# Kernel tuning notes

Measured on AMD Instinct MI355X. Metric: run time of the kernel, lower is better.

Reference implementation:

```python
import jax, jax.numpy as jnp
import numpy as np

N_NODES = 100000
N_EDGES = 1500000
N_REL = 3
HID = 256


def setup_inputs() -> dict:
    key = jax.random.key(0)
    ks = jax.random.split(key, 8)
    return {
        "feat_a": jax.random.normal(ks[0], (N_NODES, 256), dtype=jnp.float32),
        "feat_b": jax.random.normal(ks[1], (N_NODES, 384), dtype=jnp.float32),
        "Wp_a": jax.random.normal(ks[2], (256, HID), dtype=jnp.float32) * 0.03,
        "Wp_b": jax.random.normal(ks[3], (384, HID), dtype=jnp.float32) * 0.03,
        "Wr": jax.random.normal(ks[4], (N_REL, HID, HID), dtype=jnp.float32) * 0.06,
        "ln_gamma": jnp.ones((HID,), dtype=jnp.float32),
        "ln_beta": jnp.zeros((HID,), dtype=jnp.float32),
        "edge_weight": jax.random.uniform(ks[5], (N_EDGES,), dtype=jnp.float32),
        "edge_src": jax.random.randint(ks[6], (N_EDGES,), 0, N_NODES, dtype=jnp.int32),
        "edge_dst": jax.random.randint(ks[7], (N_EDGES,), 0, N_NODES, dtype=jnp.int32),
    }


def _layer_norm(x, gamma, beta, eps=1e-5):
    mu = jnp.mean(x, axis=-1, keepdims=True)
    var = jnp.mean(jnp.square(x - mu), axis=-1, keepdims=True)
    return (x - mu) * jax.lax.rsqrt(var + eps) * gamma + beta


def reference(feat_a, feat_b, Wp_a, Wp_b, Wr, ln_gamma, ln_beta,
              edge_weight, edge_src, edge_dst):
    # avg fusion of modality projections (bias-free linears), padding node zeroed
    h0 = 0.5 * (feat_a @ Wp_a + feat_b @ Wp_b)  # [N, H]
    h0 = h0.at[0].set(0.0)

    n = h0.shape[0]
    e_per_rel = edge_src.shape[0] // N_REL  # edges pre-sorted by relation id
    aggregated = jnp.zeros_like(h0)
    for r in range(N_REL):
        s = slice(r * e_per_rel, (r + 1) * e_per_rel)
        src, dst, w = edge_src[s], edge_dst[s], edge_weight[s]
        # gather -> relation linear -> weight scale  [E_r, H]
        msg = (h0[src] @ Wr[r]) * w[:, None]
        num = jax.ops.segment_sum(msg, dst, num_segments=n)
        den = jax.ops.segment_sum(w, dst, num_segments=n)
        aggregated = aggregated + num / jnp.maximum(den, 1e-8)[:, None]

    # dropout p=0 / eval -> identity; residual + LayerNorm, padding node zeroed
    h1 = _layer_norm(h0 + aggregated, ln_gamma, ln_beta)
    h1 = h1.at[0].set(0.0)
    return h1
```

## Files before the change

### kernel.cpp

```cpp
#include <hip/hip_runtime.h>

#define N_NODES 100000
#define HID 256
#define N_EDGES 1500000
#define N_REL 3
#define E_PER_REL (N_EDGES / N_REL)
#define NKEYS (N_REL * N_NODES)
#define KP 640
#define KR 768

#define SCAN_CHUNK 1024
#define NSCANBLK ((NKEYS + SCAN_CHUNK - 1) / SCAN_CHUNK)

typedef __attribute__((ext_vector_type(8))) short bf16x8;
typedef __attribute__((ext_vector_type(4))) float f32x4;

__device__ __forceinline__ short f2bf(float x) {
    union { float f; unsigned u; } v; v.f = x;
    unsigned r = v.u + 0x7fffu + ((v.u >> 16) & 1u);
    return (short)(r >> 16);
}
__device__ __forceinline__ float bf2f(short h) {
    union { unsigned u; float f; } v;
    v.u = ((unsigned)(unsigned short)h) << 16;
    return v.f;
}
__device__ __forceinline__ int xorf(int r) { return (r & 3) ^ ((r >> 2) & 3); }

__device__ __forceinline__ void gload16(const void* g, void* l) {
    typedef const __attribute__((address_space(1))) unsigned int gq;
    typedef __attribute__((address_space(3))) unsigned int lq;
    __builtin_amdgcn_global_load_lds((gq*)g, (lq*)l, 16, 0, 0);
}

__global__ __launch_bounds__(256) void wprep_kernel(
    const float* __restrict__ Wa, const float* __restrict__ Wb,
    const float* __restrict__ Wr,
    short* __restrict__ WTp, short* __restrict__ WTr)
{
    int idx = blockIdx.x * 256 + threadIdx.x;
    if (idx < 256 * KP) {
        int c = idx / KP, k = idx - c * KP;
        float v = (k < 256) ? Wa[k * HID + c] : Wb[(k - 256) * HID + c];
        WTp[idx] = f2bf(0.5f * v);
    } else {
        int j = idx - 256 * KP;
        if (j < 256 * KR) {
            int c = j / KR, k = j - c * KR;
            WTr[j] = f2bf(Wr[(k >> 8) * HID * HID + (k & 255) * HID + c]);
        }
    }
}

__global__ __launch_bounds__(512, 2) void proj_gemm(
    const float* __restrict__ fa, const float* __restrict__ fb,
    const short* __restrict__ WTp,
    unsigned char* __restrict__ h0q, float* __restrict__ h0scale)
{
    __shared__ alignas(16) char lds[147456];
    const int tid = threadIdx.x;
    const int lane = tid & 63;
    const int w = tid >> 6;
    const int wr = w >> 1, wc = w & 1;
    const int brow = blockIdx.x * 256;

    auto bufA = [&](int b) -> char* { return lds + b * 49152; };
    auto bufB = [&](int b) -> char* { return lds + b * 49152 + 32768; };

    f32x4 acc[4][8] = {};

    const int a_r8 = lane >> 3;
    const int a_sl = (lane & 7) ^ a_r8;
    int aRowG[4];
    #pragma unroll
    for (int ii = 0; ii < 4; ++ii) {
        int i = w * 4 + ii;
        int gr = brow + i * 8 + a_r8;
        aRowG[ii] = (gr < N_NODES) ? gr : (N_NODES - 1);
    }
    const int b_c16 = lane >> 2;
    int bColL[2], bSl[2];
    #pragma unroll
    for (int ii = 0; ii < 2; ++ii) {
        int i = w * 2 + ii;
        bColL[ii] = i * 16 + b_c16;
        bSl[ii] = (lane & 3) ^ xorf(bColL[ii]);
    }

    auto stage = [&](int b, int k0) {
        const float* asrc; int astr, kk;
        if (k0 < 256) { asrc = fa; astr = 256; kk = k0; }
        else          { asrc = fb; astr = 384; kk = k0 - 256; }
        #pragma unroll
        for (int ii = 0; ii < 4; ++ii) {
            int i = w * 4 + ii;
            gload16(asrc + (size_t)aRowG[ii] * astr + kk + a_sl * 4,
                    bufA(b) + i * 1024);
        }
        #pragma unroll
        for (int ii = 0; ii < 2; ++ii) {
            int i = w * 2 + ii;
            gload16(WTp + (size_t)bColL[ii] * KP + k0 + bSl[ii] * 8,
                    bufB(b) + i * 1024);
        }
    };

    const int nt = KP / 32;
    stage(0, 0); stage(1, 32); stage(2, 64);
    int cur = 0;
    for (int t = 0; t < nt; ++t) {
        if (t < nt - 2)       asm volatile("s_waitcnt vmcnt(12)" ::: "memory");
        else if (t == nt - 2) asm volatile("s_waitcnt vmcnt(6)" ::: "memory");
        else                  asm volatile("s_waitcnt vmcnt(0)" ::: "memory");
        __builtin_amdgcn_s_barrier();

        bf16x8 afr[4], bfr[8];
        #pragma unroll
        for (int m = 0; m < 4; ++m) {
            int rt = wr * 64 + m * 16 + (lane & 15);
            int p0 = (((lane >> 4) << 1) | 0) ^ (rt & 7);
            int p1 = (((lane >> 4) << 1) | 1) ^ (rt & 7);
            f32x4 lo = *(const f32x4*)(bufA(cur) + rt * 128 + p0 * 16);
            f32x4 hi = *(const f32x4*)(bufA(cur) + rt * 128 + p1 * 16);
            union { bf16x8 h; unsigned u[4]; } cv;
            asm("v_cvt_pk_bf16_f32 %0, %1, %2" : "=v"(cv.u[0]) : "v"(lo.x), "v"(lo.y));
            asm("v_cvt_pk_bf16_f32 %0, %1, %2" : "=v"(cv.u[1]) : "v"(lo.z), "v"(lo.w));
            asm("v_cvt_pk_bf16_f32 %0, %1, %2" : "=v"(cv.u[2]) : "v"(hi.x), "v"(hi.y));
            asm("v_cvt_pk_bf16_f32 %0, %1, %2" : "=v"(cv.u[3]) : "v"(hi.z), "v"(hi.w));
            afr[m] = cv.h;
        }
        #pragma unroll
        for (int n = 0; n < 8; ++n) {
            int ct = wc * 128 + n * 16 + (lane & 15);
            int p = (lane >> 4) ^ xorf(ct);
            bfr[n] = *(const bf16x8*)(bufB(cur) + ct * 64 + p * 16);
        }
        #pragma unroll
        for (int m = 0; m < 4; ++m)
            #pragma unroll
            for (int n = 0; n < 8; ++n)
                acc[m][n] = __builtin_amdgcn_mfma_f32_16x16x32_bf16(
                    afr[m], bfr[n], acc[m][n], 0, 0, 0);

        asm volatile("s_waitcnt lgkmcnt(0)" ::: "memory");
        __builtin_amdgcn_sched_barrier(0);
        __builtin_amdgcn_s_barrier();
        if (t + 3 < nt) stage(cur, (t + 3) * 32);
        cur = (cur == 2) ? 0 : cur + 1;
    }

    float* redM  = (float*)lds;
    float* smInv = redM + 512;
    #pragma unroll
    for (int m = 0; m < 4; ++m) {
        #pragma unroll
        for (int j = 0; j < 4; ++j) {
            int lrow = wr * 64 + m * 16 + ((lane >> 4) << 2) + j;
            float mx = 0.f;
            #pragma unroll
            for (int n = 0; n < 8; ++n) mx = fmaxf(mx, fabsf(acc[m][n][j]));
            #pragma unroll
            for (int off = 1; off < 16; off <<= 1)
                mx = fmaxf(mx, __shfl_xor(mx, off, 64));
            if ((lane & 15) == 0) redM[lrow * 2 + wc] = mx;
        }
    }
    __syncthreads();
    if (tid < 256) {
        float rm = fmaxf(redM[tid * 2 + 0], redM[tid * 2 + 1]);
        int grow = brow + tid;
        smInv[tid] = (rm > 0.f) ? 127.0f / rm : 0.f;
        if (grow < N_NODES)
            h0scale[grow] = (grow == 0) ? 0.f : rm * (1.0f / 127.0f);
    }
    __syncthreads();

    #pragma unroll
    for (int m = 0; m < 4; ++m) {
        #pragma unroll
        for (int j = 0; j < 4; ++j) {
            int lrow = wr * 64 + m * 16 + ((lane >> 4) << 2) + j;
            int row = brow + lrow;
            if (row >= N_NODES) continue;
            float inv = smInv[lrow];
            #pragma unroll
            for (int n = 0; n < 8; ++n) {
                int col = wc * 128 + n * 16 + (lane & 15);
                int qi = (row == 0) ? 0 : (int)rintf(acc[m][n][j] * inv);
                h0q[(size_t)row * HID + col] = (unsigned char)(signed char)qi;
            }
        }
    }
}

__global__ __launch_bounds__(512, 4) void rel_gemm_ln(
    const short* __restrict__ S, const short* __restrict__ WTr,
    const unsigned char* __restrict__ h0q, const float* __restrict__ h0scale,
    const float* __restrict__ gamma, const float* __restrict__ beta,
    float* __restrict__ out)
{
    __shared__ alignas(16) char lds[73728];
    const int tid = threadIdx.x;
    const int lane = tid & 63;
    const int w = tid >> 6;
    const int wr = w >> 2, wc = w & 3;
    const int brow = blockIdx.x * 128;

    auto bufA = [&](int b) -> char* { return lds + b * 24576; };
    auto bufB = [&](int b) -> char* { return lds + b * 24576 + 8192; };

    f32x4 acc[4][4] = {};

    const int s_r16 = lane >> 2;
    const int sRowL = w * 16 + s_r16;
    int gr0 = brow + sRowL;
    const int sRowG = (gr0 < N_NODES) ? gr0 : (N_NODES - 1);
    const int sSl = (lane & 3) ^ xorf(sRowL);
    const int b_c16 = lane >> 2;
    int bColL[2], bSl[2];
    #pragma unroll
    for (int ii = 0; ii < 2; ++ii) {
        int i = w * 2 + ii;
        bColL[ii] = i * 16 + b_c16;
        bSl[ii] = (lane & 3) ^ xorf(bColL[ii]);
    }

    auto stage = [&](int b, int k0) {
        gload16(S + (size_t)sRowG * KR + k0 + sSl * 8, bufA(b) + w * 1024);
        #pragma unroll
        for (int ii = 0; ii < 2; ++ii) {
            int i = w * 2 + ii;
            gload16(WTr + (size_t)bColL[ii] * KR + k0 + bSl[ii] * 8,
                    bufB(b) + i * 1024);
        }
    };

    const int nt = KR / 32;
    stage(0, 0); stage(1, 32); stage(2, 64);
    int cur = 0;
    for (int t = 0; t < nt; ++t) {
        if (t < nt - 2)       asm volatile("s_waitcnt vmcnt(6)" ::: "memory");
        else if (t == nt - 2) asm volatile("s_waitcnt vmcnt(3)" ::: "memory");
        else                  asm volatile("s_waitcnt vmcnt(0)" ::: "memory");
        __builtin_amdgcn_s_barrier();

        bf16x8 afr[4], bfr[4];
        #pragma unroll
        for (int m = 0; m < 4; ++m) {
            int rt = wr * 64 + m * 16 + (lane & 15);
            int p = (lane >> 4) ^ xorf(rt);
            afr[m] = *(const bf16x8*)(bufA(cur) + rt * 64 + p * 16);
        }
        #pragma unroll
        for (int n = 0; n < 4; ++n) {
            int ct = wc * 64 + n * 16 + (lane & 15);
            int p = (lane >> 4) ^ xorf(ct);
            bfr[n] = *(const bf16x8*)(bufB(cur) + ct * 64 + p * 16);
        }
        #pragma unroll
        for (int m = 0; m < 4; ++m)
            #pragma unroll
            for (int n = 0; n < 4; ++n)
                acc[m][n] = __builtin_amdgcn_mfma_f32_16x16x32_bf16(
                    afr[m], bfr[n], acc[m][n], 0, 0, 0);

        asm volatile("s_waitcnt lgkmcnt(0)" ::: "memory");
        __builtin_amdgcn_sched_barrier(0);
        __builtin_amdgcn_s_barrier();
        if (t + 3 < nt) stage(cur, (t + 3) * 32);
        cur = (cur == 2) ? 0 : cur + 1;
    }

    float* redS  = (float*)lds;
    float* redS2 = redS + 512;
    float* smMean = redS2 + 512;
    float* smRs   = smMean + 128;

    float gk[4], bk[4];
    #pragma unroll
    for (int n = 0; n < 4; ++n) {
        int col = wc * 64 + n * 16 + (lane & 15);
        gk[n] = gamma[col];
        bk[n] = beta[col];
    }

    #pragma unroll
    for (int m = 0; m < 4; ++m) {
        #pragma unroll
        for (int j = 0; j < 4; ++j) {
            int lrow = wr * 64 + m * 16 + ((lane >> 4) << 2) + j;
            int grow = brow + lrow;
            int crow = (grow < N_NODES) ? grow : 0;
            float sc = h0scale[crow];
            float s = 0.f, s2 = 0.f;
            #pragma unroll
            for (int n = 0; n < 4; ++n) {
                int col = wc * 64 + n * 16 + (lane & 15);
                float hq = (float)(int)(signed char)h0q[(size_t)crow * HID + col];
                float x = acc[m][n][j] + hq * sc;
                acc[m][n][j] = x;
                s += x; s2 = fmaf(x, x, s2);
            }
            #pragma unroll
            for (int off = 1; off < 16; off <<= 1) {
                s += __shfl_xor(s, off, 64);
                s2 += __shfl_xor(s2, off, 64);
            }
            if ((lane & 15) == 0) { redS[lrow * 4 + wc] = s; redS2[lrow * 4 + wc] = s2; }
        }
    }
    __syncthreads();
    if (tid < 128) {
        float tot  = redS[tid * 4 + 0] + redS[tid * 4 + 1] + redS[tid * 4 + 2] + redS[tid * 4 + 3];
        float tot2 = redS2[tid * 4 + 0] + redS2[tid * 4 + 1] + redS2[tid * 4 + 2] + redS2[tid * 4 + 3];
        float mean = tot * (1.0f / HID);
        float var = tot2 * (1.0f / HID) - mean * mean;
        smMean[tid] = mean;
        smRs[tid] = rsqrtf(var + 1e-5f);
    }
    __syncthreads();
    #pragma unroll
    for (int m = 0; m < 4; ++m) {
        #pragma unroll
        for (int j = 0; j < 4; ++j) {
            int lrow = wr * 64 + m * 16 + ((lane >> 4) << 2) + j;
            int grow = brow + lrow;
            if (grow >= N_NODES) continue;
            float mean = smMean[lrow], rs = smRs[lrow];
            #pragma unroll
            for (int n = 0; n < 4; ++n) {
                int col = wc * 64 + n * 16 + (lane & 15);
                float y = (acc[m][n][j] - mean) * rs * gk[n] + bk[n];
                out[(size_t)grow * HID + col] = (grow == 0) ? 0.f : y;
            }
        }
    }
}

__global__ __launch_bounds__(256) void hist_kernel(
    const int* __restrict__ dst, int* __restrict__ count)
{
    int i = blockIdx.x * 256 + threadIdx.x;
    if (i >= N_EDGES) return;
    int r = i / E_PER_REL;
    atomicAdd(&count[r * N_NODES + dst[i]], 1);
}

__global__ __launch_bounds__(256) void scan1_kernel(
    const int* __restrict__ count, int* __restrict__ offset,
    int* __restrict__ bsum)
{
    __shared__ int tmp[256];
    const int t = threadIdx.x;
    const int base = blockIdx.x * SCAN_CHUNK + t * 4;
    int v[4];
    #pragma unroll
    for (int j = 0; j < 4; ++j)
        v[j] = (base + j < NKEYS) ? count[base + j] : 0;
    int tsum = v[0] + v[1] + v[2] + v[3];
    tmp[t] = tsum;
    __syncthreads();
    #pragma unroll
    for (int off = 1; off < 256; off <<= 1) {
        int x = (t >= off) ? tmp[t - off] : 0;
        __syncthreads();
        tmp[t] += x;
        __syncthreads();
    }
    int run = tmp[t] - tsum;
    #pragma unroll
    for (int j = 0; j < 4; ++j) {
        if (base + j < NKEYS) offset[base + j] = run;
        run += v[j];
    }
    if (t == 0) bsum[blockIdx.x] = tmp[255];
}

__global__ __launch_bounds__(256) void scan2_kernel(int* __restrict__ bsum)
{
    __shared__ int tmp[256];
    const int t = threadIdx.x;
    int v0 = (2 * t     < NSCANBLK) ? bsum[2 * t]     : 0;
    int v1 = (2 * t + 1 < NSCANBLK) ? bsum[2 * t + 1] : 0;
    int psum = v0 + v1;
    tmp[t] = psum;
    __syncthreads();
    #pragma unroll
    for (int off = 1; off < 256; off <<= 1) {
        int x = (t >= off) ? tmp[t - off] : 0;
        __syncthreads();
        tmp[t] += x;
        __syncthreads();
    }
    int excl = tmp[t] - psum;
    if (2 * t     < NSCANBLK) bsum[2 * t]     = excl;
    if (2 * t + 1 < NSCANBLK) bsum[2 * t + 1] = excl + v0;
}

__global__ __launch_bounds__(256) void scan3_kernel(
    int* __restrict__ offset, const int* __restrict__ bsum)
{
    int i = blockIdx.x * 256 + threadIdx.x;
    if (i >= NKEYS) return;
    offset[i] += bsum[i / SCAN_CHUNK];
}

__global__ __launch_bounds__(256) void fill_kernel(
    const int* __restrict__ src, const int* __restrict__ dst,
    const float* __restrict__ w, const float* __restrict__ h0scale,
    int* __restrict__ offset, int4* __restrict__ csr4)
{
    int i = blockIdx.x * 256 + threadIdx.x;
    if (i >= N_EDGES) return;
    int r = i / E_PER_REL;
    int key = r * N_NODES + dst[i];
    int pos = atomicAdd(&offset[key], 1);
    int s = src[i];
    float wt = w[i];
    float ws = wt * h0scale[s];
    csr4[pos] = make_int4(s, __float_as_int(wt), __float_as_int(ws), 0);
}

__global__ __launch_bounds__(256) void gather_kernel(
    const unsigned char* __restrict__ h0q,
    const int* __restrict__ ends, const int* __restrict__ count,
    const int4* __restrict__ csr4,
    short* __restrict__ S)
{
    int gw = (blockIdx.x * 256 + threadIdx.x) >> 6;
    int lane = threadIdx.x & 63;
    if (gw >= N_REL * N_NODES) return;
    int r = gw / N_NODES;
    int node = gw - r * N_NODES;
    int deg = count[gw];
    int end = ends[gw];
    int start = end - deg;
    const int colo = lane * 4;

    float a0 = 0.f, a1 = 0.f, a2 = 0.f, a3 = 0.f;
    float den = 0.f;

    if (deg > 0) {
        int degc = (deg < 64) ? deg : 64;
        int4 e = csr4[start + ((lane < degc) ? lane : 0)];
        int msrc = e.x;
        float mw = (lane < degc) ? __int_as_float(e.y) : 0.f;
        int mws = (lane < degc) ? e.z : 0;

        float d = mw;
        #pragma unroll
        for (int off = 1; off < 64; off <<= 1) d += __shfl_xor(d, off, 64);
        den = d;

        int p = 0;
        for (; p + 4 <= degc; p += 4) {
            #pragma unroll
            for (int j = 0; j < 4; ++j) {
                int q = p + j;
                int sj = __builtin_amdgcn_readlane(msrc, q);
                float wsj = __int_as_float(__builtin_amdgcn_readlane(mws, q));
                unsigned qv = *(const unsigned*)(h0q + (size_t)sj * HID + colo);
                a0 = fmaf(wsj, (float)(int)(signed char)(qv & 255u), a0);
                a1 = fmaf(wsj, (float)(int)(signed char)((qv >> 8) & 255u), a1);
                a2 = fmaf(wsj, (float)(int)(signed char)((qv >> 16) & 255u), a2);
                a3 = fmaf(wsj, (float)(int)(signed char)(qv >> 24), a3);
            }
        }
        for (; p < degc; ++p) {
            int sj = __builtin_amdgcn_readlane(msrc, p);
            float wsj = __int_as_float(__builtin_amdgcn_readlane(mws, p));
            unsigned qv = *(const unsigned*)(h0q + (size_t)sj * HID + colo);
            a0 = fmaf(wsj, (float)(int)(signed char)(qv & 255u), a0);
            a1 = fmaf(wsj, (float)(int)(signed char)((qv >> 8) & 255u), a1);
            a2 = fmaf(wsj, (float)(int)(signed char)((qv >> 16) & 255u), a2);
            a3 = fmaf(wsj, (float)(int)(signed char)(qv >> 24), a3);
        }
        for (int pp = start + 64; pp < end; ++pp) {
            int4 ee = csr4[pp];
            float wt = __int_as_float(ee.y);
            float wsj = __int_as_float(ee.z);
            unsigned qv = *(const unsigned*)(h0q + (size_t)ee.x * HID + colo);
            a0 = fmaf(wsj, (float)(int)(signed char)(qv & 255u), a0);
            a1 = fmaf(wsj, (float)(int)(signed char)((qv >> 8) & 255u), a1);
            a2 = fmaf(wsj, (float)(int)(signed char)((qv >> 16) & 255u), a2);
            a3 = fmaf(wsj, (float)(int)(signed char)(qv >> 24), a3);
            den += wt;
        }
    }

    float inv = 1.0f / fmaxf(den, 1e-8f);
    short4 o;
    o.x = f2bf(a0 * inv);
    o.y = f2bf(a1 * inv);
    o.z = f2bf(a2 * inv);
    o.w = f2bf(a3 * inv);
    *(short4*)(S + (size_t)node * KR + r * HID + colo) = o;
}

extern "C" void kernel_launch(void* const* d_in, const int* in_sizes, int n_in,
                              void* d_out, int out_size, void* d_ws, size_t ws_size,
                              hipStream_t stream) {
    const float* fa    = (const float*)d_in[0];
    const float* fb    = (const float*)d_in[1];
    const float* Wa    = (const float*)d_in[2];
    const float* Wb    = (const float*)d_in[3];
    const float* Wr    = (const float*)d_in[4];
    const float* gamma = (const float*)d_in[5];
    const float* beta  = (const float*)d_in[6];
    const float* ew    = (const float*)d_in[7];
    const int*   esrc  = (const int*)d_in[8];
    const int*   edst  = (const int*)d_in[9];
    float* out = (float*)d_out;

    char* ws = (char*)d_ws;
    size_t off = 0;
    short* S       = (short*)(ws + off); off += (size_t)N_NODES * KR * 2;
    short* WTp     = (short*)(ws + off); off += (size_t)256 * KP * 2;
    short* WTr     = (short*)(ws + off); off += (size_t)256 * KR * 2;
    int*   count   = (int*)  (ws + off); off += (size_t)NKEYS * 4;
    int*   offs    = (int*)  (ws + off); off += (size_t)NKEYS * 4;
    int*   bsum    = (int*)  (ws + off); off += 4096;
    int4*  csr4    = (int4*) (ws + off); off += (size_t)N_EDGES * 16;
    unsigned char* h0q = (unsigned char*)(ws + off); off += (size_t)N_NODES * HID;
    float* h0scale = (float*)(ws + off); off += (size_t)N_NODES * 4;

    wprep_kernel<<<(256 * KP + 256 * KR) / 256, 256, 0, stream>>>(
        Wa, Wb, Wr, WTp, WTr);

    const int ngridP = (N_NODES + 255) / 256;
    proj_gemm<<<ngridP, 512, 0, stream>>>(fa, fb, WTp, h0q, h0scale);

    hipMemsetAsync(count, 0, (size_t)NKEYS * 4, stream);
    const int egrid = (N_EDGES + 255) / 256;
    hist_kernel<<<egrid, 256, 0, stream>>>(edst, count);
    scan1_kernel<<<NSCANBLK, 256, 0, stream>>>(count, offs, bsum);
    scan2_kernel<<<1, 256, 0, stream>>>(bsum);
    scan3_kernel<<<(NKEYS + 255) / 256, 256, 0, stream>>>(offs, bsum);
    fill_kernel<<<egrid, 256, 0, stream>>>(esrc, edst, ew, h0scale, offs, csr4);

    gather_kernel<<<(N_REL * N_NODES * 64) / 256, 256, 0, stream>>>(
        h0q, offs, count, csr4, S);

    const int ngridR = (N_NODES + 127) / 128;
    rel_gemm_ln<<<ngridR, 512, 0, stream>>>(S, WTr, h0q, h0scale, gamma, beta, out);
}
```

Measured before the change: 474.2 us.

## Quantize aggregated messages and relation weights to int8 for i8 MFMA GEMM

```diff
diff --git a/kernel.cpp b/kernel.cpp
--- a/kernel.cpp
+++ b/kernel.cpp
@@ -14,17 +14,13 @@
 
 typedef __attribute__((ext_vector_type(8))) short bf16x8;
 typedef __attribute__((ext_vector_type(4))) float f32x4;
+typedef __attribute__((ext_vector_type(4))) int   i32x4;
 
 __device__ __forceinline__ short f2bf(float x) {
     union { float f; unsigned u; } v; v.f = x;
     unsigned r = v.u + 0x7fffu + ((v.u >> 16) & 1u);
     return (short)(r >> 16);
 }
-__device__ __forceinline__ float bf2f(short h) {
-    union { unsigned u; float f; } v;
-    v.u = ((unsigned)(unsigned short)h) << 16;
-    return v.f;
-}
 __device__ __forceinline__ int xorf(int r) { return (r & 3) ^ ((r >> 2) & 3); }
 
 __device__ __forceinline__ void gload16(const void* g, void* l) {
@@ -35,21 +31,43 @@
 
 __global__ __launch_bounds__(256) void wprep_kernel(
     const float* __restrict__ Wa, const float* __restrict__ Wb,
-    const float* __restrict__ Wr,
-    short* __restrict__ WTp, short* __restrict__ WTr)
+    short* __restrict__ WTp)
 {
     int idx = blockIdx.x * 256 + threadIdx.x;
     if (idx < 256 * KP) {
         int c = idx / KP, k = idx - c * KP;
         float v = (k < 256) ? Wa[k * HID + c] : Wb[(k - 256) * HID + c];
         WTp[idx] = f2bf(0.5f * v);
-    } else {
-        int j = idx - 256 * KP;
-        if (j < 256 * KR) {
-            int c = j / KR, k = j - c * KR;
-            WTr[j] = f2bf(Wr[(k >> 8) * HID * HID + (k & 255) * HID + c]);
-        }
-    }
+    }
+}
+
+__global__ __launch_bounds__(256) void wprep2_kernel(
+    const float* __restrict__ Wr,
+    signed char* __restrict__ WTrq, float* __restrict__ sB)
+{
+    __shared__ float red[4];
+    const int c = blockIdx.x;
+    const int tid = threadIdx.x;
+    const int lane = tid & 63;
+    float v[3];
+    float mx = 0.f;
+    #pragma unroll
+    for (int j = 0; j < 3; ++j) {
+        int k = tid * 3 + j;
+        v[j] = Wr[(k >> 8) * (HID * HID) + (k & 255) * HID + c];
+        mx = fmaxf(mx, fabsf(v[j]));
+    }
+    #pragma unroll
+    for (int off = 1; off < 64; off <<= 1)
+        mx = fmaxf(mx, __shfl_xor(mx, off, 64));
+    if (lane == 0) red[tid >> 6] = mx;
+    __syncthreads();
+    mx = fmaxf(fmaxf(red[0], red[1]), fmaxf(red[2], red[3]));
+    if (tid == 0) sB[c] = mx * (1.0f / 127.0f);
+    float qinv = (mx > 0.f) ? 127.0f / mx : 0.f;
+    #pragma unroll
+    for (int j = 0; j < 3; ++j)
+        WTrq[(size_t)c * KR + tid * 3 + j] = (signed char)(int)rintf(v[j] * qinv);
 }
 
 __global__ __launch_bounds__(512, 2) void proj_gemm(
@@ -194,12 +212,14 @@
 }
 
 __global__ __launch_bounds__(512, 4) void rel_gemm_ln(
-    const short* __restrict__ S, const short* __restrict__ WTr,
+    const unsigned char* __restrict__ Sq, const signed char* __restrict__ WTrq,
+    const float* __restrict__ sSg, const float* __restrict__ sB,
     const unsigned char* __restrict__ h0q, const float* __restrict__ h0scale,
     const float* __restrict__ gamma, const float* __restrict__ beta,
     float* __restrict__ out)
 {
     __shared__ alignas(16) char lds[73728];
+    __shared__ float sS_lds[384];
     const int tid = threadIdx.x;
     const int lane = tid & 63;
     const int w = tid >> 6;
@@ -209,7 +229,15 @@
     auto bufA = [&](int b) -> char* { return lds + b * 24576; };
     auto bufB = [&](int b) -> char* { return lds + b * 24576 + 8192; };
 
-    f32x4 acc[4][4] = {};
+    if (tid < 128) {
+        int gr = brow + tid;
+        if (gr >= N_NODES) gr = N_NODES - 1;
+        #pragma unroll
+        for (int j = 0; j < 3; ++j) sS_lds[tid * 3 + j] = sSg[gr * 3 + j];
+    }
+
+    i32x4 acci[4][4] = {};
+    f32x4 accf[4][4] = {};
 
     const int s_r16 = lane >> 2;
     const int sRowL = w * 16 + s_r16;
@@ -226,17 +254,17 @@
     }
 
     auto stage = [&](int b, int k0) {
-        gload16(S + (size_t)sRowG * KR + k0 + sSl * 8, bufA(b) + w * 1024);
+        gload16(Sq + (size_t)sRowG * KR + k0 + sSl * 16, bufA(b) + w * 1024);
         #pragma unroll
         for (int ii = 0; ii < 2; ++ii) {
             int i = w * 2 + ii;
-            gload16(WTr + (size_t)bColL[ii] * KR + k0 + bSl[ii] * 8,
+            gload16(WTrq + (size_t)bColL[ii] * KR + k0 + bSl[ii] * 16,
                     bufB(b) + i * 1024);
         }
     };
 
-    const int nt = KR / 32;
-    stage(0, 0); stage(1, 32); stage(2, 64);
+    const int nt = KR / 64;
+    stage(0, 0); stage(1, 64); stage(2, 128);
     int cur = 0;
     for (int t = 0; t < nt; ++t) {
         if (t < nt - 2)       asm volatile("s_waitcnt vmcnt(6)" ::: "memory");
@@ -244,30 +272,46 @@
         else                  asm volatile("s_waitcnt vmcnt(0)" ::: "memory");
         __builtin_amdgcn_s_barrier();
 
-        bf16x8 afr[4], bfr[4];
+        i32x4 afr[4], bfr[4];
         #pragma unroll
         for (int m = 0; m < 4; ++m) {
             int rt = wr * 64 + m * 16 + (lane & 15);
             int p = (lane >> 4) ^ xorf(rt);
-            afr[m] = *(const bf16x8*)(bufA(cur) + rt * 64 + p * 16);
+            afr[m] = *(const i32x4*)(bufA(cur) + rt * 64 + p * 16);
         }
         #pragma unroll
         for (int n = 0; n < 4; ++n) {
             int ct = wc * 64 + n * 16 + (lane & 15);
             int p = (lane >> 4) ^ xorf(ct);
-            bfr[n] = *(const bf16x8*)(bufB(cur) + ct * 64 + p * 16);
+            bfr[n] = *(const i32x4*)(bufB(cur) + ct * 64 + p * 16);
         }
         #pragma unroll
         for (int m = 0; m < 4; ++m)
             #pragma unroll
             for (int n = 0; n < 4; ++n)
-                acc[m][n] = __builtin_amdgcn_mfma_f32_16x16x32_bf16(
-                    afr[m], bfr[n], acc[m][n], 0, 0, 0);
+                acci[m][n] = __builtin_amdgcn_mfma_i32_16x16x64_i8(
+                    afr[m], bfr[n], acci[m][n], 0, 0, 0);
+
+        if ((t & 3) == 3) {
+            int seg = t >> 2;
+            #pragma unroll
+            for (int m = 0; m < 4; ++m)
+                #pragma unroll
+                for (int j = 0; j < 4; ++j) {
+                    int lrow = wr * 64 + m * 16 + ((lane >> 4) << 2) + j;
+                    float sc = sS_lds[lrow * 3 + seg];
+                    #pragma unroll
+                    for (int n = 0; n < 4; ++n) {
+                        accf[m][n][j] = fmaf(sc, (float)acci[m][n][j], accf[m][n][j]);
+                        acci[m][n][j] = 0;
+                    }
+                }
+        }
 
         asm volatile("s_waitcnt lgkmcnt(0)" ::: "memory");
         __builtin_amdgcn_sched_barrier(0);
         __builtin_amdgcn_s_barrier();
-        if (t + 3 < nt) stage(cur, (t + 3) * 32);
+        if (t + 3 < nt) stage(cur, (t + 3) * 64);
         cur = (cur == 2) ? 0 : cur + 1;
     }
 
@@ -276,14 +320,16 @@
     float* smMean = redS2 + 512;
     float* smRs   = smMean + 128;
 
-    float gk[4], bk[4];
+    float gk[4], bk[4], sbv[4];
     #pragma unroll
     for (int n = 0; n < 4; ++n) {
         int col = wc * 64 + n * 16 + (lane & 15);
         gk[n] = gamma[col];
         bk[n] = beta[col];
-    }
-
+        sbv[n] = sB[col];
+    }
+
+    __syncthreads();
     #pragma unroll
     for (int m = 0; m < 4; ++m) {
         #pragma unroll
@@ -297,8 +343,8 @@
             for (int n = 0; n < 4; ++n) {
                 int col = wc * 64 + n * 16 + (lane & 15);
                 float hq = (float)(int)(signed char)h0q[(size_t)crow * HID + col];
-                float x = acc[m][n][j] + hq * sc;
-                acc[m][n][j] = x;
+                float x = accf[m][n][j] * sbv[n] + hq * sc;
+                accf[m][n][j] = x;
                 s += x; s2 = fmaf(x, x, s2);
             }
             #pragma unroll
@@ -330,7 +376,7 @@
             #pragma unroll
             for (int n = 0; n < 4; ++n) {
                 int col = wc * 64 + n * 16 + (lane & 15);
-                float y = (acc[m][n][j] - mean) * rs * gk[n] + bk[n];
+                float y = (accf[m][n][j] - mean) * rs * gk[n] + bk[n];
                 out[(size_t)grow * HID + col] = (grow == 0) ? 0.f : y;
             }
         }
@@ -425,7 +471,7 @@
     const unsigned char* __restrict__ h0q,
     const int* __restrict__ ends, const int* __restrict__ count,
     const int4* __restrict__ csr4,
-    short* __restrict__ S)
+    unsigned char* __restrict__ Sq, float* __restrict__ sSg)
 {
     int gw = (blockIdx.x * 256 + threadIdx.x) >> 6;
     int lane = threadIdx.x & 63;
@@ -489,12 +535,21 @@
     }
 
     float inv = 1.0f / fmaxf(den, 1e-8f);
-    short4 o;
-    o.x = f2bf(a0 * inv);
-    o.y = f2bf(a1 * inv);
-    o.z = f2bf(a2 * inv);
-    o.w = f2bf(a3 * inv);
-    *(short4*)(S + (size_t)node * KR + r * HID + colo) = o;
+    float av0 = a0 * inv, av1 = a1 * inv, av2 = a2 * inv, av3 = a3 * inv;
+
+    float mx = fmaxf(fmaxf(fabsf(av0), fabsf(av1)), fmaxf(fabsf(av2), fabsf(av3)));
+    #pragma unroll
+    for (int off = 1; off < 64; off <<= 1)
+        mx = fmaxf(mx, __shfl_xor(mx, off, 64));
+    float qinv = (mx > 0.f) ? 127.0f / mx : 0.f;
+    int q0 = (int)rintf(av0 * qinv);
+    int q1 = (int)rintf(av1 * qinv);
+    int q2 = (int)rintf(av2 * qinv);
+    int q3 = (int)rintf(av3 * qinv);
+    unsigned packed = (unsigned)(q0 & 255) | ((unsigned)(q1 & 255) << 8)
+                    | ((unsigned)(q2 & 255) << 16) | ((unsigned)(q3 & 255) << 24);
+    *(unsigned*)(Sq + (size_t)node * KR + r * HID + colo) = packed;
+    if (lane == 0) sSg[node * 3 + r] = mx * (1.0f / 127.0f);
 }
 
 extern "C" void kernel_launch(void* const* d_in, const int* in_sizes, int n_in,
@@ -514,18 +569,20 @@
 
     char* ws = (char*)d_ws;
     size_t off = 0;
-    short* S       = (short*)(ws + off); off += (size_t)N_NODES * KR * 2;
-    short* WTp     = (short*)(ws + off); off += (size_t)256 * KP * 2;
-    short* WTr     = (short*)(ws + off); off += (size_t)256 * KR * 2;
-    int*   count   = (int*)  (ws + off); off += (size_t)NKEYS * 4;
-    int*   offs    = (int*)  (ws + off); off += (size_t)NKEYS * 4;
-    int*   bsum    = (int*)  (ws + off); off += 4096;
-    int4*  csr4    = (int4*) (ws + off); off += (size_t)N_EDGES * 16;
-    unsigned char* h0q = (unsigned char*)(ws + off); off += (size_t)N_NODES * HID;
-    float* h0scale = (float*)(ws + off); off += (size_t)N_NODES * 4;
-
-    wprep_kernel<<<(256 * KP + 256 * KR) / 256, 256, 0, stream>>>(
-        Wa, Wb, Wr, WTp, WTr);
+    unsigned char* Sq   = (unsigned char*)(ws + off); off += (size_t)N_NODES * KR;
+    short* WTp          = (short*)(ws + off);        off += (size_t)256 * KP * 2;
+    signed char* WTrq   = (signed char*)(ws + off);  off += (size_t)256 * KR;
+    float* sB           = (float*)(ws + off);        off += 256 * 4;
+    int*   count        = (int*)(ws + off);          off += (size_t)NKEYS * 4;
+    int*   offs         = (int*)(ws + off);          off += (size_t)NKEYS * 4;
+    int*   bsum         = (int*)(ws + off);          off += 4096;
+    int4*  csr4         = (int4*)(ws + off);         off += (size_t)N_EDGES * 16;
+    unsigned char* h0q  = (unsigned char*)(ws + off); off += (size_t)N_NODES * HID;
+    float* h0scale      = (float*)(ws + off);        off += (size_t)N_NODES * 4;
+    float* sSg          = (float*)(ws + off);        off += (size_t)N_NODES * 3 * 4;
+
+    wprep_kernel<<<(256 * KP) / 256, 256, 0, stream>>>(Wa, Wb, WTp);
+    wprep2_kernel<<<256, 256, 0, stream>>>(Wr, WTrq, sB);
 
     const int ngridP = (N_NODES + 255) / 256;
     proj_gemm<<<ngridP, 512, 0, stream>>>(fa, fb, WTp, h0q, h0scale);
@@ -539,8 +596,9 @@
     fill_kernel<<<egrid, 256, 0, stream>>>(esrc, edst, ew, h0scale, offs, csr4);
 
     gather_kernel<<<(N_REL * N_NODES * 64) / 256, 256, 0, stream>>>(
-        h0q, offs, count, csr4, S);
+        h0q, offs, count, csr4, Sq, sSg);
 
     const int ngridR = (N_NODES + 127) / 128;
-    rel_gemm_ln<<<ngridR, 512, 0, stream>>>(S, WTr, h0q, h0scale, gamma, beta, out);
-}
+    rel_gemm_ln<<<ngridR, 512, 0, stream>>>(
+        Sq, WTrq, sSg, sB, h0q, h0scale, gamma, beta, out);
+}
```

Result: slower. 516.5 us (+8.9%).
